# Performance work log

Hardware: AMD Instinct MI355X
Metric: run time of the kernel (lower is better)

Reference implementation:

```python
import jax, jax.numpy as jnp
import numpy as np

B, L, D, NC, H = 2, 192, 768, 4, 256  # batch, seq_len, bert_hidden, num_case(+coref), hidden


def setup_inputs() -> dict:
    key = jax.random.key(0)
    ks = jax.random.split(key, 9)
    s = 0.02  # init scale
    return {
        "sequence_output": jax.random.normal(ks[0], (B, L, D), dtype=jnp.float32),
        "base_score": jax.random.normal(ks[1], (B, L, NC, L), dtype=jnp.float32),
        "Wp": jax.random.normal(ks[2], (D, H), dtype=jnp.float32) * s,
        "bp": jnp.zeros((H,), dtype=jnp.float32),
        "Wa": jax.random.normal(ks[3], (D, NC * H), dtype=jnp.float32) * s,
        "ba": jnp.zeros((NC * H,), dtype=jnp.float32),
        "Wmid": jax.random.normal(ks[4], (NC, H + NC, H), dtype=jnp.float32) * s,
        "bmid": jnp.zeros((NC, H), dtype=jnp.float32),
        "Wout": jax.random.normal(ks[5], (NC, H), dtype=jnp.float32) * s,
    }


def reference(sequence_output, base_score, Wp, bp, Wa, ba, Wmid, bmid, Wout):
    b, l, d = sequence_output.shape
    nc = Wmid.shape[0]
    h = Wp.shape[1]
    # dropout is identity in eval mode
    h_p = sequence_output @ Wp + bp                       # [B, L, H] (predicate)
    h_a = (sequence_output @ Wa + ba).reshape(b, l, nc, h)  # [B, L, NC, H] (argument)
    # broadcast add: predicate axis p, argument axis a -> [B, P, A, NC, H]
    h_pa = jnp.tanh(h_p[:, :, None, None, :] + h_a[:, None, :, :, :])
    # base_score [B, L, NC, L] -> transpose(2,3) -> [B, P, A, NC], expand over case axis
    bs = jnp.swapaxes(base_score, 2, 3)                   # [B, P, A, NC]
    bs = jnp.broadcast_to(bs[:, :, :, None, :], (b, l, l, nc, nc))
    hcat = jnp.concatenate([h_pa, bs], axis=-1)           # [B, P, A, NC, H+NC]
    # per-case mid Linear, batched as a single einsum over the case axis n
    h_mid = jnp.tanh(jnp.einsum('bpanc,nch->bpanh', hcat, Wmid) + bmid)
    out = jnp.einsum('bpanh,nh->bpan', h_mid, Wout)       # [B, P, A, NC]
    return jnp.transpose(out, (0, 1, 3, 2))               # [B, P, NC, A]
```

## Files before the change

### kernel.cpp

```cpp
#include <hip/hip_runtime.h>

#define LSEQ 192
#define DIM  768
#define NCASE 4
#define HID  256
#define BATCH 2

#define TANH_K 2.885390081777927f

typedef float  floatx4 __attribute__((ext_vector_type(4)));
typedef __bf16 bf16x8  __attribute__((ext_vector_type(8)));
typedef __bf16 bf16x4  __attribute__((ext_vector_type(4)));

__device__ __forceinline__ float tanh_pre(float x) {
    float e = __builtin_amdgcn_exp2f(x);
    return 1.0f - 2.0f * __builtin_amdgcn_rcpf(e + 1.0f);
}

__device__ __forceinline__ float tanh_add(float tu, float tv) {
    float den = __builtin_fmaf(tu, tv, 1.0f);
    return (tu + tv) * __builtin_amdgcn_rcpf(den);
}

__device__ __forceinline__ void barrier_lds_only() {
    __builtin_amdgcn_sched_barrier(0);
    __builtin_amdgcn_s_waitcnt(0xC07F);
    __builtin_amdgcn_s_barrier();
    __builtin_amdgcn_sched_barrier(0);
}

template <int CTRL>
__device__ __forceinline__ float dpp_add(float v) {
    int x = __builtin_amdgcn_update_dpp(0, __builtin_bit_cast(int, v),
                                        CTRL, 0xF, 0xF, true);
    return v + __builtin_bit_cast(float, x);
}
__device__ __forceinline__ float row16_reduce(float v) {
    v = dpp_add<0xB1>(v);
    v = dpp_add<0x4E>(v);
    v = dpp_add<0x141>(v);
    v = dpp_add<0x140>(v);
    return v;
}


__global__ __launch_bounds__(256) void prep(
    const float* __restrict__ seq, const float* __restrict__ Wp,
    const float* __restrict__ Wa,  const float* __restrict__ bp,
    const float* __restrict__ ba,  const float* __restrict__ Wmid,
    const float* __restrict__ bmid,
    float* __restrict__ lin, bf16x8* __restrict__ Bpack)
{
    const int blk = blockIdx.x;
    const int tid = threadIdx.x;

    if (blk >= 1920) {
        int u = (blk - 1920) * 256 + tid;
        int lane = u & 63, f = u >> 6;
        int ct = f & 15, nk = f >> 4;
        int kc = nk % 9, n = nk / 9;
        int h = ct * 16 + (lane & 15);
        int kbase = kc * 32 + ((lane >> 4) & 3) * 8;
        bf16x8 v;
        #pragma unroll
        for (int j = 0; j < 8; j++) {
            int k = kbase + j;
            float x;
            if (k < 260)       x = Wmid[(size_t)(n * 260 + k) * 256 + h];
            else if (k == 260) x = bmid[n * 256 + h];
            else               x = 0.0f;
            v[j] = (__bf16)(TANH_K * x);
        }
        Bpack[u] = v;
        return;
    }

    const int w = tid >> 6, lane = tid & 63;
    const int rt = blk / 80, cg = blk % 80;
    const int quad  = lane >> 4;
    const int col16 = lane & 15;

    __shared__ float cmb[3][256];

    const int arow = rt * 16 + col16;
    const int col  = cg * 16 + col16;
    const int kofs = w * 192;
    const float* aptr = seq + (size_t)arow * DIM + kofs + quad * 8;
    const float* wbase = (cg < 16) ? (Wp + col) : (Wa + (col - 256));
    const int    wstr  = (cg < 16) ? HID : (NCASE * HID);

    floatx4 acc = {};
    floatx4 a0 = *(const floatx4*)(aptr);
    floatx4 a1 = *(const floatx4*)(aptr + 4);
    float bv[8];
    #pragma unroll
    for (int j = 0; j < 8; j++)
        bv[j] = wbase[(size_t)(kofs + quad * 8 + j) * wstr];

    #pragma unroll
    for (int kc = 0; kc < 6; kc++) {
        bf16x8 ah, al, bh, bl;
        #pragma unroll
        for (int j = 0; j < 4; j++) {
            __bf16 h0 = (__bf16)a0[j];
            ah[j] = h0; al[j] = (__bf16)(a0[j] - (float)h0);
            __bf16 h1 = (__bf16)a1[j];
            ah[4 + j] = h1; al[4 + j] = (__bf16)(a1[j] - (float)h1);
        }
        #pragma unroll
        for (int j = 0; j < 8; j++) {
            __bf16 h = (__bf16)bv[j];
            bh[j] = h; bl[j] = (__bf16)(bv[j] - (float)h);
        }
        if (kc < 5) {
            a0 = *(const floatx4*)(aptr + (kc + 1) * 32);
            a1 = *(const floatx4*)(aptr + (kc + 1) * 32 + 4);
            #pragma unroll
            for (int j = 0; j < 8; j++)
                bv[j] = wbase[(size_t)(kofs + (kc + 1) * 32 + quad * 8 + j) * wstr];
        }
        acc = __builtin_amdgcn_mfma_f32_16x16x32_bf16(ah, bh, acc, 0, 0, 0);
        acc = __builtin_amdgcn_mfma_f32_16x16x32_bf16(al, bh, acc, 0, 0, 0);
        acc = __builtin_amdgcn_mfma_f32_16x16x32_bf16(ah, bl, acc, 0, 0, 0);
    }

    if (w > 0) *(floatx4*)&cmb[w - 1][lane * 4] = acc;
    __syncthreads();
    if (w == 0) {
        #pragma unroll
        for (int i = 0; i < 3; i++) {
            floatx4 p = *(const floatx4*)&cmb[i][lane * 4];
            acc += p;
        }
        const float bias = (cg < 16) ? bp[col] : ba[col - 256];
        #pragma unroll
        for (int reg = 0; reg < 4; reg++)
            lin[(size_t)(rt * 16 + quad * 4 + reg) * 1280 + col] =
                tanh_pre(TANH_K * (acc[reg] + bias));
    }
}

__global__ __launch_bounds__(512, 6) void refine_main(
    const float* __restrict__ lin,
    const float* __restrict__ base_score,
    const float* __restrict__ Wout,
    const bf16x8* __restrict__ Bpack,
    float* __restrict__ out)
{
    const int bx = blockIdx.x;
    const int n  = blockIdx.y;
    const int b  = blockIdx.z;
    const int ptile = bx / 24, atile = bx % 24;
    const int p0 = ptile * 8, a0r = atile * 8;

    const int tid   = threadIdx.x;
    const int w     = tid >> 6;
    const int lane  = tid & 63;
    const int quad  = lane >> 4;
    const int col16 = lane & 15;

    __shared__ __align__(16) __bf16 A0[256 * 8];
    __shared__ __align__(16) __bf16 A1[256 * 8];
    __shared__ float red[8][64];

    const int s_g    = tid >> 1;
    const int h2     = tid & 1;
    const int l_g    = s_g & 63;
    const int m_gen  = ((s_g >> 6) << 4) + (l_g & 15);
    const int kq     = (l_g >> 4) * 8 + h2 * 4;
    const int quad_g = l_g >> 4;

    const int pg = p0 + (m_gen >> 3), ag = a0r + (m_gen & 7);
    const float* hp_ptr = lin + (size_t)(b * LSEQ + pg) * 1280 + kq;
    const float* ha_ptr = lin + (size_t)(b * LSEQ + ag) * 1280 + 256 + n * 256 + kq;

    const bf16x8* bbase = Bpack + ((size_t)(n * 9) * 16 + w * 2) * 64 + lane;

    float bs4[4] = {};
    if (quad_g == 0 && h2 == 0) {
        #pragma unroll
        for (int j = 0; j < 4; j++)
            bs4[j] = base_score[((size_t)(b * LSEQ + pg) * NCASE + j) * LSEQ + ag];
    }
    float wo[2];
    #pragma unroll
    for (int ct = 0; ct < 2; ct++)
        wo[ct] = Wout[n * 256 + w * 32 + ct * 16 + col16];

    bf16x8 bcur[2];
    #pragma unroll
    for (int ct = 0; ct < 2; ct++) bcur[ct] = bbase[ct * 64];

    floatx4 hp = *(const floatx4*)(hp_ptr);
    floatx4 ha = *(const floatx4*)(ha_ptr);
    {
        bf16x4 av;
        #pragma unroll
        for (int j = 0; j < 4; j++) av[j] = (__bf16)tanh_add(hp[j], ha[j]);
        *(bf16x4*)&A0[tid * 4] = av;
    }
    hp = *(const floatx4*)(hp_ptr + 32);
    ha = *(const floatx4*)(ha_ptr + 32);
    barrier_lds_only();

    floatx4 acc[4][2] = {};

    #pragma unroll
    for (int kc = 0; kc < 9; kc++) {
        bf16x8 bnext[2];
        if (kc < 8) {
            #pragma unroll
            for (int ct = 0; ct < 2; ct++)
                bnext[ct] = bbase[((kc + 1) * 16 + ct) * 64];
        }
        if (kc < 7) {
            floatx4 u0 = hp, v0 = ha;
            if (kc < 6) {
                hp = *(const floatx4*)(hp_ptr + (kc + 2) * 32);
                ha = *(const floatx4*)(ha_ptr + (kc + 2) * 32);
            }
            bf16x4 av;
            #pragma unroll
            for (int j = 0; j < 4; j++) av[j] = (__bf16)tanh_add(u0[j], v0[j]);
            __bf16* buf = ((kc + 1) & 1) ? A1 : A0;
            *(bf16x4*)&buf[tid * 4] = av;
        } else if (kc == 7) {
            bf16x4 av = {};
            if (quad_g == 0) {
                if (h2 == 0) {
                    #pragma unroll
                    for (int j = 0; j < 4; j++) av[j] = (__bf16)bs4[j];
                } else {
                    av[0] = (__bf16)1.0f;
                }
            }
            *(bf16x4*)&A0[tid * 4] = av;
        }

        const __bf16* rb = (kc & 1) ? A1 : A0;
        bf16x8 af[4];
        #pragma unroll
        for (int rt = 0; rt < 4; rt++)
            af[rt] = *(const bf16x8*)&rb[(rt * 64 + lane) * 8];
        #pragma unroll
        for (int rt = 0; rt < 4; rt++)
            #pragma unroll
            for (int ct = 0; ct < 2; ct++)
                acc[rt][ct] = __builtin_amdgcn_mfma_f32_16x16x32_bf16(
                    af[rt], bcur[ct], acc[rt][ct], 0, 0, 0);
        #pragma unroll
        for (int ct = 0; ct < 2; ct++) bcur[ct] = bnext[ct];
        if (kc < 8) barrier_lds_only();
    }

    #pragma unroll
    for (int rt = 0; rt < 4; rt++) {
        #pragma unroll
        for (int reg = 0; reg < 4; reg++) {
            float rs = tanh_pre(acc[rt][0][reg]) * wo[0]
                     + tanh_pre(acc[rt][1][reg]) * wo[1];
            rs = row16_reduce(rs);
            if (col16 == 0) red[w][rt * 16 + quad * 4 + reg] = rs;
        }
    }
    barrier_lds_only();

    if (tid < 64) {
        float total = red[0][tid] + red[1][tid] + red[2][tid] + red[3][tid]
                    + red[4][tid] + red[5][tid] + red[6][tid] + red[7][tid];
        const int p = p0 + (tid >> 3), a = a0r + (tid & 7);
        out[((size_t)(b * LSEQ + p) * NCASE + n) * LSEQ + a] = total;
    }
}

extern "C" void kernel_launch(void* const* d_in, const int* in_sizes, int n_in,
                              void* d_out, int out_size, void* d_ws, size_t ws_size,
                              hipStream_t stream) {
    const float* seq  = (const float*)d_in[0];
    const float* bsc  = (const float*)d_in[1];
    const float* Wp   = (const float*)d_in[2];
    const float* bp   = (const float*)d_in[3];
    const float* Wa   = (const float*)d_in[4];
    const float* ba   = (const float*)d_in[5];
    const float* Wmid = (const float*)d_in[6];
    const float* bmid = (const float*)d_in[7];
    const float* Wout = (const float*)d_in[8];
    float* out = (float*)d_out;

    char* ws = (char*)d_ws;
    float*  lin   = (float*)(ws);
    bf16x8* Bpack = (bf16x8*)(ws + 1966080);

    prep<<<2064, 256, 0, stream>>>(seq, Wp, Wa, bp, ba, Wmid, bmid, lin, Bpack);
    refine_main<<<dim3(576, NCASE, BATCH), 512, 0, stream>>>(
        lin, bsc, Wout, Bpack, out);
}
```

Before: 148.4 us.

## Process two K-chunks per LDS phase to halve barriers in refine_main

Restructures the main K loop of refine_main from nine 32-wide chunks, each with its own barrier, into four phases that each stage two chunks in a larger double buffer, plus a separate final fold chunk (base_score and bias). The goal is to halve the number of workgroup barriers and give the scheduler more independent MFMA work between syncs. In exchange it uses more LDS and registers per block, and launch bounds are lowered from 6 to 5 blocks per SM to match. B fragments are now loaded at the start of each phase instead of being prefetched one step ahead, which may expose global load latency.

After: 155.0 us. 4.4% more time.

```diff
diff --git a/kernel.cpp b/kernel.cpp
--- a/kernel.cpp
+++ b/kernel.cpp
@@ -140,7 +140,7 @@
     }
 }
 
-__global__ __launch_bounds__(512, 6) void refine_main(
+__global__ __launch_bounds__(512, 5) void refine_main(
     const float* __restrict__ lin,
     const float* __restrict__ base_score,
     const float* __restrict__ Wout,
@@ -159,8 +159,8 @@
     const int quad  = lane >> 4;
     const int col16 = lane & 15;
 
-    __shared__ __align__(16) __bf16 A0[256 * 8];
-    __shared__ __align__(16) __bf16 A1[256 * 8];
+    __shared__ __align__(16) __bf16 Abuf[2][4096];
+    __shared__ __align__(16) __bf16 Afold[2048];
     __shared__ float red[8][64];
 
     const int s_g    = tid >> 1;
@@ -187,44 +187,55 @@
     for (int ct = 0; ct < 2; ct++)
         wo[ct] = Wout[n * 256 + w * 32 + ct * 16 + col16];
 
-    bf16x8 bcur[2];
-    #pragma unroll
-    for (int ct = 0; ct < 2; ct++) bcur[ct] = bbase[ct * 64];
-
-    floatx4 hp = *(const floatx4*)(hp_ptr);
-    floatx4 ha = *(const floatx4*)(ha_ptr);
+    floatx4 hpA = *(const floatx4*)(hp_ptr);
+    floatx4 haA = *(const floatx4*)(ha_ptr);
+    floatx4 hpB = *(const floatx4*)(hp_ptr + 32);
+    floatx4 haB = *(const floatx4*)(ha_ptr + 32);
     {
-        bf16x4 av;
-        #pragma unroll
-        for (int j = 0; j < 4; j++) av[j] = (__bf16)tanh_add(hp[j], ha[j]);
-        *(bf16x4*)&A0[tid * 4] = av;
-    }
-    hp = *(const floatx4*)(hp_ptr + 32);
-    ha = *(const floatx4*)(ha_ptr + 32);
+        bf16x4 avA, avB;
+        #pragma unroll
+        for (int j = 0; j < 4; j++) {
+            avA[j] = (__bf16)tanh_add(hpA[j], haA[j]);
+            avB[j] = (__bf16)tanh_add(hpB[j], haB[j]);
+        }
+        *(bf16x4*)&Abuf[0][tid * 4]        = avA;
+        *(bf16x4*)&Abuf[0][2048 + tid * 4] = avB;
+    }
+    hpA = *(const floatx4*)(hp_ptr + 64);
+    haA = *(const floatx4*)(ha_ptr + 64);
+    hpB = *(const floatx4*)(hp_ptr + 96);
+    haB = *(const floatx4*)(ha_ptr + 96);
     barrier_lds_only();
 
     floatx4 acc[4][2] = {};
 
     #pragma unroll
-    for (int kc = 0; kc < 9; kc++) {
-        bf16x8 bnext[2];
-        if (kc < 8) {
+    for (int ph = 0; ph < 4; ph++) {
+        bf16x8 bv[2][2];
+        #pragma unroll
+        for (int c = 0; c < 2; c++)
             #pragma unroll
             for (int ct = 0; ct < 2; ct++)
-                bnext[ct] = bbase[((kc + 1) * 16 + ct) * 64];
-        }
-        if (kc < 7) {
-            floatx4 u0 = hp, v0 = ha;
-            if (kc < 6) {
-                hp = *(const floatx4*)(hp_ptr + (kc + 2) * 32);
-                ha = *(const floatx4*)(ha_ptr + (kc + 2) * 32);
+                bv[c][ct] = bbase[((2 * ph + c) * 16 + ct) * 64];
+
+        if (ph < 3) {
+            floatx4 uA = hpA, vA = haA, uB = hpB, vB = haB;
+            if (ph < 2) {
+                hpA = *(const floatx4*)(hp_ptr + (2 * ph + 4) * 32);
+                haA = *(const floatx4*)(ha_ptr + (2 * ph + 4) * 32);
+                hpB = *(const floatx4*)(hp_ptr + (2 * ph + 5) * 32);
+                haB = *(const floatx4*)(ha_ptr + (2 * ph + 5) * 32);
             }
-            bf16x4 av;
-            #pragma unroll
-            for (int j = 0; j < 4; j++) av[j] = (__bf16)tanh_add(u0[j], v0[j]);
-            __bf16* buf = ((kc + 1) & 1) ? A1 : A0;
-            *(bf16x4*)&buf[tid * 4] = av;
-        } else if (kc == 7) {
+            bf16x4 avA, avB;
+            #pragma unroll
+            for (int j = 0; j < 4; j++) {
+                avA[j] = (__bf16)tanh_add(uA[j], vA[j]);
+                avB[j] = (__bf16)tanh_add(uB[j], vB[j]);
+            }
+            __bf16* buf = Abuf[(ph + 1) & 1];
+            *(bf16x4*)&buf[tid * 4]        = avA;
+            *(bf16x4*)&buf[2048 + tid * 4] = avB;
+        } else {
             bf16x4 av = {};
             if (quad_g == 0) {
                 if (h2 == 0) {
@@ -234,23 +245,40 @@
                     av[0] = (__bf16)1.0f;
                 }
             }
-            *(bf16x4*)&A0[tid * 4] = av;
-        }
-
-        const __bf16* rb = (kc & 1) ? A1 : A0;
+            *(bf16x4*)&Afold[tid * 4] = av;
+        }
+
+        const __bf16* rb = Abuf[ph & 1];
+        #pragma unroll
+        for (int c = 0; c < 2; c++) {
+            bf16x8 af[4];
+            #pragma unroll
+            for (int rt = 0; rt < 4; rt++)
+                af[rt] = *(const bf16x8*)&rb[c * 2048 + (rt * 64 + lane) * 8];
+            #pragma unroll
+            for (int rt = 0; rt < 4; rt++)
+                #pragma unroll
+                for (int ct = 0; ct < 2; ct++)
+                    acc[rt][ct] = __builtin_amdgcn_mfma_f32_16x16x32_bf16(
+                        af[rt], bv[c][ct], acc[rt][ct], 0, 0, 0);
+        }
+        barrier_lds_only();
+    }
+
+    {
+        bf16x8 bf[2];
+        #pragma unroll
+        for (int ct = 0; ct < 2; ct++) bf[ct] = bbase[(8 * 16 + ct) * 64];
         bf16x8 af[4];
         #pragma unroll
         for (int rt = 0; rt < 4; rt++)
-            af[rt] = *(const bf16x8*)&rb[(rt * 64 + lane) * 8];
+            af[rt] = *(const bf16x8*)&Afold[(rt * 64 + lane) * 8];
         #pragma unroll
         for (int rt = 0; rt < 4; rt++)
             #pragma unroll
             for (int ct = 0; ct < 2; ct++)
                 acc[rt][ct] = __builtin_amdgcn_mfma_f32_16x16x32_bf16(
-                    af[rt], bcur[ct], acc[rt][ct], 0, 0, 0);
-        #pragma unroll
-        for (int ct = 0; ct < 2; ct++) bcur[ct] = bnext[ct];
-        if (kc < 8) barrier_lds_only();
+                    af[rt], bf[ct], acc[rt][ct], 0, 0, 0);
     }
 
     #pragma unroll
```
